# Kernel tuning notes

Measured on AMD Instinct MI355X. Metric: run time of the kernel, lower is better.

Reference implementation:

```python
import math
import jax, jax.numpy as jnp
import numpy as np

L, H, D, FF, V, S = 12, 12, 768, 3072, 32000, 1024
HD = D // H
EPS = 1e-5
B, T = 2, 1024


def layernorm(x, w, b):
    mu = jnp.mean(x, axis=-1, keepdims=True)
    var = jnp.mean(jnp.square(x - mu), axis=-1, keepdims=True)
    return (x - mu) * jax.lax.rsqrt(var + EPS) * w + b


def setup_inputs() -> dict:
    key = jax.random.key(0)
    ks = jax.random.split(key, 12)
    std = 0.02
    std_res = 0.02 / math.sqrt(2 * L)  # out_proj / down_proj scaled init
    return {
        "input_ids": jax.random.randint(ks[0], (B, T), 0, V),
        "tok_emb": jax.random.normal(ks[1], (V, D), jnp.float32) * std,
        "pos_emb": jax.random.normal(ks[2], (S, D), jnp.float32) * std,
        "ln1_w": jnp.ones((L, D), jnp.float32),
        "ln1_b": jnp.zeros((L, D), jnp.float32),
        "qkv_w": jax.random.normal(ks[3], (L, 3 * D, D), jnp.float32) * std,
        "out_w": jax.random.normal(ks[4], (L, D, D), jnp.float32) * std_res,
        "ln2_w": jnp.ones((L, D), jnp.float32),
        "ln2_b": jnp.zeros((L, D), jnp.float32),
        "up_w": jax.random.normal(ks[5], (L, FF, D), jnp.float32) * std,
        "down_w": jax.random.normal(ks[6], (L, D, FF), jnp.float32) * std_res,
        "lnf_w": jnp.ones((D,), jnp.float32),
        "lnf_b": jnp.zeros((D,), jnp.float32),
    }


def reference(input_ids, tok_emb, pos_emb, ln1_w, ln1_b, qkv_w, out_w,
              ln2_w, ln2_b, up_w, down_w, lnf_w, lnf_b):
    b, t = input_ids.shape
    x = tok_emb[input_ids] + pos_emb[:t]  # (B,T,D); dropout = eval no-op
    causal = jnp.tril(jnp.ones((t, t), bool))  # (T,T)
    scale = 1.0 / math.sqrt(HD)

    def block(x, p):
        l1w, l1b, qkvw, ow, l2w, l2b, uw, dw = p
        h = layernorm(x, l1w, l1b)
        qkv = h @ qkvw.T  # (B,T,3D)
        q, k, v = jnp.split(qkv, 3, axis=-1)
        q = q.reshape(b, t, H, HD)
        k = k.reshape(b, t, H, HD)
        v = v.reshape(b, t, H, HD)
        scores = jnp.einsum('bihd,bjhd->bhij', q, k) * scale
        scores = jnp.where(causal, scores, -jnp.inf)
        probs = jax.nn.softmax(scores, axis=-1)  # attn_dropout = eval no-op
        o = jnp.einsum('bhij,bjhd->bihd', probs, v).reshape(b, t, D)
        x = x + o @ ow.T
        h2 = layernorm(x, l2w, l2b)
        x = x + jax.nn.gelu(h2 @ uw.T, approximate=False) @ dw.T
        return x, None

    x, _ = jax.lax.scan(block, x, (ln1_w, ln1_b, qkv_w, out_w, ln2_w, ln2_b, up_w, down_w))
    x = layernorm(x, lnf_w, lnf_b)
    logits = x @ tok_emb.T  # tied lm_head
    return logits
```

## Files before the change

kernel.cpp:

```cpp
#include <hip/hip_runtime.h>
#include <hip/hip_bf16.h>
#include <math.h>

#define L_  12
#define H_  12
#define D_  768
#define FF_ 3072
#define V_  32000
#define T_  1024
#define B_  2
#define BT_ (B_*T_)

typedef unsigned short ushort_t;
typedef unsigned int   uint_t;
typedef __bf16 bf16x8 __attribute__((ext_vector_type(8)));
typedef float  f32x4  __attribute__((ext_vector_type(4)));

__device__ __forceinline__ uint_t f2bf1(float f) {
    uint_t u = __builtin_bit_cast(uint_t, f);
    return (u + 0x7FFFu + ((u >> 16) & 1u)) >> 16;
}
__device__ __forceinline__ uint_t f2bf2(float lo, float hi) {
    return f2bf1(lo) | (f2bf1(hi) << 16);
}

__device__ __forceinline__ void gl_lds16(const ushort_t* g, ushort_t* l) {
    __builtin_amdgcn_global_load_lds(
        (const __attribute__((address_space(1))) uint_t*)g,
        (__attribute__((address_space(3))) uint_t*)l, 16, 0, 0);
}

__global__ __launch_bounds__(256) void cast_bf16(const float* __restrict__ in,
                                                 ushort_t* __restrict__ out, int n8)
{
    for (int i = blockIdx.x * 256 + threadIdx.x; i < n8; i += gridDim.x * 256) {
        const float4* p = (const float4*)(in + (size_t)i * 8);
        float4 a = p[0], b = p[1];
        *(uint4*)(out + (size_t)i * 8) =
            make_uint4(f2bf2(a.x,a.y), f2bf2(a.z,a.w), f2bf2(b.x,b.y), f2bf2(b.z,b.w));
    }
}

#define EPI_F32   0
#define EPI_BF16  1
#define EPI_GELU  2
#define EPI_PART  3

template <int EPI, int BM, int KS>
__global__ __launch_bounds__(256) void gemm_bt(
    const ushort_t* __restrict__ A, const ushort_t* __restrict__ W,
    const float* R, void* Cv, int N, int K, int Kc)
{
    constexpr int MI = BM / 32;
    constexpr int AH = BM * 32;
    constexpr int BH = 128 * 32;
    __shared__ ushort_t As[2 * AH];
    __shared__ ushort_t Bs[2 * BH];

    const int tid  = threadIdx.x;
    const int w    = tid >> 6;
    const int lane = tid & 63;

    const int nwg = gridDim.x;
    int swz = (blockIdx.x & 7) * (nwg >> 3) + (blockIdx.x >> 3);
    constexpr int MT = 2048 / BM;
    const int mt = swz & (MT - 1);
    int rest     = swz / MT;
    const int ks = rest & (KS - 1);
    const int nt = rest / KS;
    const int m0 = mt * BM, n0 = nt * 128;
    const int kb = ks * Kc;

    const int srow = lane >> 2;
    const int scol = ((lane & 3) ^ ((srow >> 1) & 3)) * 8;
    const ushort_t* gA = A + (size_t)(m0 + w * (BM / 4) + srow) * K + scol;
    const ushort_t* gW = W + (size_t)(n0 + w * 32 + srow) * K + scol;
    const size_t row16 = (size_t)16 * K;

    const int lr = lane & 15;
    const int lg = lane >> 4;
    const int wm = (w >> 1) * (BM / 2);
    const int wn = (w & 1) * 64;

    f32x4 acc[MI][4] = {};

    auto stage = [&](int buf, int k0) {
        ushort_t* lA = As + buf * AH + w * (BM / 4) * 32;
        ushort_t* lB = Bs + buf * BH + w * 1024;
        #pragma unroll
        for (int i = 0; i < BM / 64; ++i)
            gl_lds16(gA + k0 + i * row16, lA + i * 512);
        #pragma unroll
        for (int i = 0; i < 2; ++i)
            gl_lds16(gW + k0 + i * row16, lB + i * 512);
    };

    stage(0, kb);
    __syncthreads();
    int cur = 0;
    for (int k0 = kb; k0 < kb + Kc; k0 += 32) {
        if (k0 + 32 < kb + Kc) stage(cur ^ 1, k0 + 32);
        const ushort_t* Ab = As + cur * AH;
        const ushort_t* Bb = Bs + cur * BH;
        __builtin_amdgcn_s_setprio(1);
        {
            bf16x8 av[MI], bv[4];
            #pragma unroll
            for (int i = 0; i < MI; ++i) {
                int rr = wm + i * 16 + lr;
                int ch = lg ^ ((rr >> 1) & 3);
                av[i] = *(const bf16x8*)&Ab[rr * 32 + ch * 8];
            }
            #pragma unroll
            for (int j = 0; j < 4; ++j) {
                int rr = wn + j * 16 + lr;
                int ch = lg ^ ((rr >> 1) & 3);
                bv[j] = *(const bf16x8*)&Bb[rr * 32 + ch * 8];
            }
            #pragma unroll
            for (int i = 0; i < MI; ++i)
                #pragma unroll
                for (int j = 0; j < 4; ++j)
                    acc[i][j] = __builtin_amdgcn_mfma_f32_16x16x32_bf16(av[i], bv[j], acc[i][j], 0, 0, 0);
        }
        __builtin_amdgcn_s_setprio(0);
        __syncthreads();
        cur ^= 1;
    }

    float*    Cf = (float*)Cv;
    ushort_t* Cb = (ushort_t*)Cv;
    float*    Pp = (EPI == EPI_PART) ? (ks ? const_cast<float*>(R) : (float*)Cv) : nullptr;
    const int rbase = lg * 4;
    #pragma unroll
    for (int i = 0; i < MI; ++i) {
        #pragma unroll
        for (int j = 0; j < 4; ++j) {
            #pragma unroll
            for (int r = 0; r < 4; ++r) {
                int row = m0 + wm + i * 16 + rbase + r;
                int col = n0 + wn + j * 16 + lr;
                size_t idx = (size_t)row * N + col;
                float v = acc[i][j][r];
                if (EPI == EPI_F32)  Cf[idx] = v;
                if (EPI == EPI_BF16) Cb[idx] = (ushort_t)f2bf1(v);
                if (EPI == EPI_GELU) Cb[idx] = (ushort_t)f2bf1(0.5f * v * (1.0f + erff(v * 0.70710678118654752f)));
                if (EPI == EPI_PART) Pp[idx] = v;
            }
        }
    }
}

__global__ __launch_bounds__(256) void vprep(const ushort_t* __restrict__ qkv,
                                             ushort_t* __restrict__ vt)
{
    __shared__ ushort_t Vs[64][72];
    const int blk   = blockIdx.x;
    const int ttile = blk & 15;
    const int bh    = blk >> 4;
    const int b     = bh / H_;
    const int h     = bh % H_;
    const int tid   = threadIdx.x;
    const int t0    = ttile * 64;
    {
        const int tr = tid >> 2;
        const int dc = (tid & 3) * 16;
        const uint4* src = (const uint4*)(qkv + (size_t)(b * T_ + t0 + tr) * 2304 + 1536 + h * 64 + dc);
        uint4 v0 = src[0], v1 = src[1];
        *(uint4*)&Vs[tr][dc]     = v0;
        *(uint4*)&Vs[tr][dc + 8] = v1;
    }
    __syncthreads();
    {
        const int d  = tid >> 2;
        const int jc = (tid & 3) * 16;
        uint_t w[8];
        #pragma unroll
        for (int i = 0; i < 8; ++i)
            w[i] = (uint_t)Vs[jc + 2*i][d] | ((uint_t)Vs[jc + 2*i + 1][d] << 16);
        uint4* dst = (uint4*)(vt + ((size_t)bh * 64 + d) * T_ + t0 + jc);
        dst[0] = make_uint4(w[0], w[1], w[2], w[3]);
        dst[1] = make_uint4(w[4], w[5], w[6], w[7]);
    }
}

__global__ __launch_bounds__(64) void attn_mfma(const ushort_t* __restrict__ qkv,
    const ushort_t* __restrict__ vt, ushort_t* __restrict__ o)
{
    __shared__ ushort_t Ps[16 * 136];

    int swz = (blockIdx.x & 7) * 192 + (blockIdx.x >> 3);
    const int bh  = swz >> 6;
    const int qtl = 63 - (swz & 63);
    const int b   = bh / H_;
    const int h   = bh % H_;
    const int lane = threadIdx.x;
    const int l15  = lane & 15;
    const int lg   = lane >> 4;
    const int qbase = qtl * 16;
    const int qlast = qbase + 15;

    const ushort_t* qp = qkv + ((size_t)(b * T_) + qbase + l15) * 2304 + h * 64 + lg * 8;
    bf16x8 qf0 = *(const bf16x8*)qp;
    bf16x8 qf1 = *(const bf16x8*)(qp + 32);

    f32x4 od[4] = {};
    float mr[4] = {-INFINITY, -INFINITY, -INFINITY, -INFINITY};
    float lr[4] = {0.f, 0.f, 0.f, 0.f};

    const ushort_t* kbase = qkv + (size_t)(b * T_) * 2304 + 768 + h * 64;
    const ushort_t* vbase = vt + (size_t)bh * 64 * T_;
    const float SC = 0.18033688011112042f;

    for (int j0 = 0; j0 <= qlast; j0 += 128) {
        f32x4 s[8];
        __builtin_amdgcn_s_setprio(1);
        #pragma unroll
        for (int n = 0; n < 8; ++n) {
            if (j0 + 16 * n <= qlast) {
                const ushort_t* kr = kbase + (size_t)(j0 + 16 * n + l15) * 2304 + lg * 8;
                bf16x8 kf0 = *(const bf16x8*)kr;
                bf16x8 kf1 = *(const bf16x8*)(kr + 32);
                f32x4 a = {};
                a = __builtin_amdgcn_mfma_f32_16x16x32_bf16(qf0, kf0, a, 0, 0, 0);
                a = __builtin_amdgcn_mfma_f32_16x16x32_bf16(qf1, kf1, a, 0, 0, 0);
                s[n] = a;
            } else {
                s[n] = f32x4{-INFINITY, -INFINITY, -INFINITY, -INFINITY};
            }
        }
        __builtin_amdgcn_s_setprio(0);

        #pragma unroll
        for (int n = 0; n < 8; ++n) {
            #pragma unroll
            for (int r = 0; r < 4; ++r) {
                float v = s[n][r] * SC;
                int jg = j0 + 16 * n + l15;
                int qg = qbase + lg * 4 + r;
                if (jg > qg) v = -INFINITY;
                s[n][r] = v;
            }
        }

        float al[4];
        #pragma unroll
        for (int r = 0; r < 4; ++r) {
            float tm = fmaxf(fmaxf(fmaxf(s[0][r], s[1][r]), fmaxf(s[2][r], s[3][r])),
                             fmaxf(fmaxf(s[4][r], s[5][r]), fmaxf(s[6][r], s[7][r])));
            tm = fmaxf(tm, __shfl_xor(tm, 1, 64));
            tm = fmaxf(tm, __shfl_xor(tm, 2, 64));
            tm = fmaxf(tm, __shfl_xor(tm, 4, 64));
            tm = fmaxf(tm, __shfl_xor(tm, 8, 64));
            float mn = fmaxf(mr[r], tm);
            al[r] = exp2f(mr[r] - mn);
            mr[r] = mn;
        }
        #pragma unroll
        for (int n = 0; n < 8; ++n)
            #pragma unroll
            for (int r = 0; r < 4; ++r)
                s[n][r] = exp2f(s[n][r] - mr[r]);
        #pragma unroll
        for (int r = 0; r < 4; ++r) {
            float ps = (s[0][r] + s[1][r]) + (s[2][r] + s[3][r]);
            ps += (s[4][r] + s[5][r]) + (s[6][r] + s[7][r]);
            ps += __shfl_xor(ps, 1, 64);
            ps += __shfl_xor(ps, 2, 64);
            ps += __shfl_xor(ps, 4, 64);
            ps += __shfl_xor(ps, 8, 64);
            lr[r] = lr[r] * al[r] + ps;
        }
        #pragma unroll
        for (int n = 0; n < 4; ++n)
            #pragma unroll
            for (int r = 0; r < 4; ++r)
                od[n][r] *= al[r];

        #pragma unroll
        for (int n = 0; n < 8; ++n)
            #pragma unroll
            for (int r = 0; r < 4; ++r)
                Ps[(lg * 4 + r) * 136 + 16 * n + l15] = (ushort_t)f2bf1(s[n][r]);

        __builtin_amdgcn_s_setprio(1);
        #pragma unroll
        for (int kc = 0; kc < 4; ++kc) {
            if (j0 + kc * 32 <= qlast) {
                bf16x8 pa = *(const bf16x8*)&Ps[l15 * 136 + kc * 32 + lg * 8];
                #pragma unroll
                for (int nn = 0; nn < 4; ++nn) {
                    bf16x8 vf = *(const bf16x8*)&vbase[(size_t)(16 * nn + l15) * T_ + j0 + kc * 32 + lg * 8];
                    od[nn] = __builtin_amdgcn_mfma_f32_16x16x32_bf16(pa, vf, od[nn], 0, 0, 0);
                }
            }
        }
        __builtin_amdgcn_s_setprio(0);
    }

    #pragma unroll
    for (int r = 0; r < 4; ++r) {
        float inv = 1.0f / lr[r];
        int row = qbase + lg * 4 + r;
        ushort_t* op = o + ((size_t)(b * T_ + row)) * 768 + h * 64 + l15;
        #pragma unroll
        for (int nn = 0; nn < 4; ++nn)
            op[16 * nn] = (ushort_t)f2bf1(od[nn][r] * inv);
    }
}

__global__ __launch_bounds__(256) void ln_kernel(const float* __restrict__ x,
    const float* __restrict__ w, const float* __restrict__ bia, ushort_t* __restrict__ out)
{
    const int row = blockIdx.x;
    const int tid = threadIdx.x;
    const float* xr = x + (size_t)row * 768;
    float v0 = xr[tid], v1 = xr[tid + 256], v2 = xr[tid + 512];
    float s  = v0 + v1 + v2;
    float s2 = v0 * v0 + v1 * v1 + v2 * v2;
    #pragma unroll
    for (int off = 32; off > 0; off >>= 1) {
        s  += __shfl_down(s,  off, 64);
        s2 += __shfl_down(s2, off, 64);
    }
    __shared__ float sh[8];
    const int wave = tid >> 6;
    if ((tid & 63) == 0) { sh[wave] = s; sh[4 + wave] = s2; }
    __syncthreads();
    float S  = sh[0] + sh[1] + sh[2] + sh[3];
    float S2 = sh[4] + sh[5] + sh[6] + sh[7];
    float mean = S * (1.f / 768.f);
    float var  = S2 * (1.f / 768.f) - mean * mean;
    float inv  = rsqrtf(var + 1e-5f);
    ushort_t* orow = out + (size_t)row * 768;
    orow[tid]       = (ushort_t)f2bf1((v0 - mean) * inv * w[tid]       + bia[tid]);
    orow[tid + 256] = (ushort_t)f2bf1((v1 - mean) * inv * w[tid + 256] + bia[tid + 256]);
    orow[tid + 512] = (ushort_t)f2bf1((v2 - mean) * inv * w[tid + 512] + bia[tid + 512]);
}

__global__ __launch_bounds__(256) void ln_red(float* __restrict__ x,
    const float* __restrict__ P0, const float* __restrict__ P1,
    const float* __restrict__ w, const float* __restrict__ bia, ushort_t* __restrict__ out)
{
    const int row = blockIdx.x;
    const int tid = threadIdx.x;
    const size_t base = (size_t)row * 768;
    float v0 = x[base + tid]       + P0[base + tid]       + P1[base + tid];
    float v1 = x[base + tid + 256] + P0[base + tid + 256] + P1[base + tid + 256];
    float v2 = x[base + tid + 512] + P0[base + tid + 512] + P1[base + tid + 512];
    x[base + tid]       = v0;
    x[base + tid + 256] = v1;
    x[base + tid + 512] = v2;
    float s  = v0 + v1 + v2;
    float s2 = v0 * v0 + v1 * v1 + v2 * v2;
    #pragma unroll
    for (int off = 32; off > 0; off >>= 1) {
        s  += __shfl_down(s,  off, 64);
        s2 += __shfl_down(s2, off, 64);
    }
    __shared__ float sh[8];
    const int wave = tid >> 6;
    if ((tid & 63) == 0) { sh[wave] = s; sh[4 + wave] = s2; }
    __syncthreads();
    float S  = sh[0] + sh[1] + sh[2] + sh[3];
    float S2 = sh[4] + sh[5] + sh[6] + sh[7];
    float mean = S * (1.f / 768.f);
    float var  = S2 * (1.f / 768.f) - mean * mean;
    float inv  = rsqrtf(var + 1e-5f);
    ushort_t* orow = out + base;
    orow[tid]       = (ushort_t)f2bf1((v0 - mean) * inv * w[tid]       + bia[tid]);
    orow[tid + 256] = (ushort_t)f2bf1((v1 - mean) * inv * w[tid + 256] + bia[tid + 256]);
    orow[tid + 512] = (ushort_t)f2bf1((v2 - mean) * inv * w[tid + 512] + bia[tid + 512]);
}

__global__ __launch_bounds__(256) void embed_kernel(const int* __restrict__ ids,
    const float* __restrict__ tok, const float* __restrict__ pos, float* __restrict__ x)
{
    const int bt = blockIdx.x;
    const int t  = bt % T_;
    const int id = ids[bt];
    const int tid = threadIdx.x;
    const float* tr = tok + (size_t)id * 768;
    const float* pr = pos + (size_t)t * 768;
    float* xr = x + (size_t)bt * 768;
    xr[tid]       = tr[tid]       + pr[tid];
    xr[tid + 256] = tr[tid + 256] + pr[tid + 256];
    xr[tid + 512] = tr[tid + 512] + pr[tid + 512];
}

extern "C" void kernel_launch(void* const* d_in, const int* in_sizes, int n_in,
                              void* d_out, int out_size, void* d_ws, size_t ws_size,
                              hipStream_t stream)
{
    const int*   ids   = (const int*)  d_in[0];
    const float* tok   = (const float*)d_in[1];
    const float* pos   = (const float*)d_in[2];
    const float* ln1w  = (const float*)d_in[3];
    const float* ln1b  = (const float*)d_in[4];
    const float* qkvw  = (const float*)d_in[5];
    const float* outw  = (const float*)d_in[6];
    const float* ln2w  = (const float*)d_in[7];
    const float* ln2b  = (const float*)d_in[8];
    const float* upw   = (const float*)d_in[9];
    const float* downw = (const float*)d_in[10];
    const float* lnfw  = (const float*)d_in[11];
    const float* lnfb  = (const float*)d_in[12];
    float* out = (float*)d_out;

    char* ws = (char*)d_ws;
    ushort_t* h    = (ushort_t*)ws;
    float*    x    = (float*)   (ws + 3145728);
    ushort_t* qkv  = (ushort_t*)(ws + 9437184);
    ushort_t* o    = qkv  + (size_t)BT_ * 3 * D_;
    ushort_t* vt   = o    + (size_t)BT_ * D_;
    ushort_t* ffh  = vt   + (size_t)B_ * H_ * 64 * T_;
    float*    Pa   = (float*)(ws + 37748736);
    float*    Pb   = (float*)(ws + 44040192);
    ushort_t* qkvwB  = (ushort_t*)(ws + 50331648);
    ushort_t* outwB  = qkvwB  + (size_t)L_ * 3 * D_ * D_;
    ushort_t* upwB   = outwB  + (size_t)L_ * D_ * D_;
    ushort_t* downwB = upwB   + (size_t)L_ * FF_ * D_;
    ushort_t* tokW   = downwB + (size_t)L_ * D_ * FF_;

    cast_bf16<<<2048, 256, 0, stream>>>(qkvw,  qkvwB,  L_ * 3 * D_ * D_ / 8);
    cast_bf16<<<2048, 256, 0, stream>>>(outw,  outwB,  L_ * D_ * D_ / 8);
    cast_bf16<<<2048, 256, 0, stream>>>(upw,   upwB,   L_ * FF_ * D_ / 8);
    cast_bf16<<<2048, 256, 0, stream>>>(downw, downwB, L_ * D_ * FF_ / 8);

    embed_kernel<<<BT_, 256, 0, stream>>>(ids, tok, pos, x);

    for (int l = 0; l < L_; ++l) {
        if (l == 0)
            ln_kernel<<<BT_, 256, 0, stream>>>(x, ln1w, ln1b, h);
        else
            ln_red<<<BT_, 256, 0, stream>>>(x, Pa, Pb, ln1w + l * D_, ln1b + l * D_, h);

        gemm_bt<EPI_BF16, 128, 1><<<16 * (3 * D_ / 128), 256, 0, stream>>>(
            h, qkvwB + (size_t)l * 3 * D_ * D_, nullptr, qkv, 3 * D_, D_, D_);

        vprep<<<B_ * H_ * (T_ / 64), 256, 0, stream>>>(qkv, vt);
        attn_mfma<<<B_ * H_ * (T_ / 16), 64, 0, stream>>>(qkv, vt, o);

        gemm_bt<EPI_PART, 64, 2><<<32 * (D_ / 128) * 2, 256, 0, stream>>>(
            o, outwB + (size_t)l * D_ * D_, Pb, Pa, D_, D_, D_ / 2);

        ln_red<<<BT_, 256, 0, stream>>>(x, Pa, Pb, ln2w + l * D_, ln2b + l * D_, h);

        gemm_bt<EPI_GELU, 128, 1><<<16 * (FF_ / 128), 256, 0, stream>>>(
            h, upwB + (size_t)l * FF_ * D_, nullptr, ffh, FF_, D_, D_);

        gemm_bt<EPI_PART, 64, 2><<<32 * (D_ / 128) * 2, 256, 0, stream>>>(
            ffh, downwB + (size_t)l * D_ * FF_, Pb, Pa, D_, FF_, FF_ / 2);
    }

    ln_red<<<BT_, 256, 0, stream>>>(x, Pa, Pb, lnfw, lnfb, h);

    cast_bf16<<<2048, 256, 0, stream>>>(tok, tokW, V_ * D_ / 8);
    gemm_bt<EPI_F32, 128, 1><<<16 * (V_ / 128), 256, 0, stream>>>(
        h, tokW, nullptr, out, V_, D_, D_);
}
```

Measured before the change: 2.234 ms.

## Fuse V transpose into QKV GEMM epilogue and cast weights per layer

The QKV GEMM gains an epilogue that writes Q and K row-major and scatters V directly into the transposed per-head layout, which removes the separate vprep kernel and its round trip through memory. The four large upfront weight casts become one fused per-layer cast into a small reused buffer, so the bf16 weights of each layer are likely still in L2 when the GEMMs read them. The QKV and up-projection GEMMs switch from BM=128 to BM=64 tiles, doubling the grid. The risks are scattered 8-byte V stores, an extra launch per layer, and more weight re-reads with smaller tiles.

After: 2.036 ms. 1.1x faster.

```diff
diff --git a/kernel.cpp b/kernel.cpp
--- a/kernel.cpp
+++ b/kernel.cpp
@@ -41,15 +41,34 @@
     }
 }
 
+__global__ __launch_bounds__(256) void cast_layer(const float* __restrict__ q,
+    const float* __restrict__ o, const float* __restrict__ u, const float* __restrict__ d,
+    ushort_t* __restrict__ out)
+{
+    const int N0 = 3*D_*D_/8, N1 = N0 + D_*D_/8, N2 = N1 + FF_*D_/8, N3 = N2 + D_*FF_/8;
+    for (int i = blockIdx.x * 256 + threadIdx.x; i < N3; i += gridDim.x * 256) {
+        const float* src;
+        if      (i < N0) src = q + (size_t)i * 8;
+        else if (i < N1) src = o + (size_t)(i - N0) * 8;
+        else if (i < N2) src = u + (size_t)(i - N1) * 8;
+        else             src = d + (size_t)(i - N2) * 8;
+        const float4* p = (const float4*)src;
+        float4 a = p[0], b = p[1];
+        *(uint4*)(out + (size_t)i * 8) =
+            make_uint4(f2bf2(a.x,a.y), f2bf2(a.z,a.w), f2bf2(b.x,b.y), f2bf2(b.z,b.w));
+    }
+}
+
 #define EPI_F32   0
 #define EPI_BF16  1
 #define EPI_GELU  2
 #define EPI_PART  3
+#define EPI_QKV   4
 
 template <int EPI, int BM, int KS>
 __global__ __launch_bounds__(256) void gemm_bt(
     const ushort_t* __restrict__ A, const ushort_t* __restrict__ W,
-    const float* R, void* Cv, int N, int K, int Kc)
+    const float* R, void* Cv, ushort_t* __restrict__ Vt, int N, int K, int Kc)
 {
     constexpr int MI = BM / 32;
     constexpr int AH = BM * 32;
@@ -136,51 +155,33 @@
     for (int i = 0; i < MI; ++i) {
         #pragma unroll
         for (int j = 0; j < 4; ++j) {
-            #pragma unroll
-            for (int r = 0; r < 4; ++r) {
-                int row = m0 + wm + i * 16 + rbase + r;
-                int col = n0 + wn + j * 16 + lr;
-                size_t idx = (size_t)row * N + col;
-                float v = acc[i][j][r];
-                if (EPI == EPI_F32)  Cf[idx] = v;
-                if (EPI == EPI_BF16) Cb[idx] = (ushort_t)f2bf1(v);
-                if (EPI == EPI_GELU) Cb[idx] = (ushort_t)f2bf1(0.5f * v * (1.0f + erff(v * 0.70710678118654752f)));
-                if (EPI == EPI_PART) Pp[idx] = v;
-            }
-        }
-    }
-}
-
-__global__ __launch_bounds__(256) void vprep(const ushort_t* __restrict__ qkv,
-                                             ushort_t* __restrict__ vt)
-{
-    __shared__ ushort_t Vs[64][72];
-    const int blk   = blockIdx.x;
-    const int ttile = blk & 15;
-    const int bh    = blk >> 4;
-    const int b     = bh / H_;
-    const int h     = bh % H_;
-    const int tid   = threadIdx.x;
-    const int t0    = ttile * 64;
-    {
-        const int tr = tid >> 2;
-        const int dc = (tid & 3) * 16;
-        const uint4* src = (const uint4*)(qkv + (size_t)(b * T_ + t0 + tr) * 2304 + 1536 + h * 64 + dc);
-        uint4 v0 = src[0], v1 = src[1];
-        *(uint4*)&Vs[tr][dc]     = v0;
-        *(uint4*)&Vs[tr][dc + 8] = v1;
-    }
-    __syncthreads();
-    {
-        const int d  = tid >> 2;
-        const int jc = (tid & 3) * 16;
-        uint_t w[8];
-        #pragma unroll
-        for (int i = 0; i < 8; ++i)
-            w[i] = (uint_t)Vs[jc + 2*i][d] | ((uint_t)Vs[jc + 2*i + 1][d] << 16);
-        uint4* dst = (uint4*)(vt + ((size_t)bh * 64 + d) * T_ + t0 + jc);
-        dst[0] = make_uint4(w[0], w[1], w[2], w[3]);
-        dst[1] = make_uint4(w[4], w[5], w[6], w[7]);
+            const int row0 = m0 + wm + i * 16 + rbase;
+            const int col  = n0 + wn + j * 16 + lr;
+            if (EPI == EPI_QKV) {
+                if (col < 1536) {
+                    #pragma unroll
+                    for (int r = 0; r < 4; ++r)
+                        Cb[(size_t)(row0 + r) * 2304 + col] = (ushort_t)f2bf1(acc[i][j][r]);
+                } else {
+                    const int hh = (col - 1536) >> 6, dd = (col - 1536) & 63;
+                    const int bb = row0 >> 10,        tt = row0 & 1023;
+                    uint2 pk;
+                    pk.x = f2bf2(acc[i][j][0], acc[i][j][1]);
+                    pk.y = f2bf2(acc[i][j][2], acc[i][j][3]);
+                    *(uint2*)&Vt[(((size_t)bb * H_ + hh) * 64 + dd) * T_ + tt] = pk;
+                }
+            } else {
+                #pragma unroll
+                for (int r = 0; r < 4; ++r) {
+                    size_t idx = (size_t)(row0 + r) * N + col;
+                    float v = acc[i][j][r];
+                    if (EPI == EPI_F32)  Cf[idx] = v;
+                    if (EPI == EPI_BF16) Cb[idx] = (ushort_t)f2bf1(v);
+                    if (EPI == EPI_GELU) Cb[idx] = (ushort_t)f2bf1(0.5f * v * (1.0f + erff(v * 0.70710678118654752f)));
+                    if (EPI == EPI_PART) Pp[idx] = v;
+                }
+            }
+        }
     }
 }
 
@@ -416,46 +417,48 @@
     ushort_t* ffh  = vt   + (size_t)B_ * H_ * 64 * T_;
     float*    Pa   = (float*)(ws + 37748736);
     float*    Pb   = (float*)(ws + 44040192);
-    ushort_t* qkvwB  = (ushort_t*)(ws + 50331648);
-    ushort_t* outwB  = qkvwB  + (size_t)L_ * 3 * D_ * D_;
-    ushort_t* upwB   = outwB  + (size_t)L_ * D_ * D_;
-    ushort_t* downwB = upwB   + (size_t)L_ * FF_ * D_;
-    ushort_t* tokW   = downwB + (size_t)L_ * D_ * FF_;
-
-    cast_bf16<<<2048, 256, 0, stream>>>(qkvw,  qkvwB,  L_ * 3 * D_ * D_ / 8);
-    cast_bf16<<<2048, 256, 0, stream>>>(outw,  outwB,  L_ * D_ * D_ / 8);
-    cast_bf16<<<2048, 256, 0, stream>>>(upw,   upwB,   L_ * FF_ * D_ / 8);
-    cast_bf16<<<2048, 256, 0, stream>>>(downw, downwB, L_ * D_ * FF_ / 8);
+    ushort_t* layerW = (ushort_t*)(ws + 50331648);
+    ushort_t* tokW   = (ushort_t*)(ws + 67108864);
+
+    ushort_t* qkvwB  = layerW;
+    ushort_t* outwB  = qkvwB + (size_t)3 * D_ * D_;
+    ushort_t* upwB   = outwB + (size_t)D_ * D_;
+    ushort_t* downwB = upwB  + (size_t)FF_ * D_;
 
     embed_kernel<<<BT_, 256, 0, stream>>>(ids, tok, pos, x);
 
     for (int l = 0; l < L_; ++l) {
+        cast_layer<<<1024, 256, 0, stream>>>(
+            qkvw  + (size_t)l * 3 * D_ * D_,
+            outw  + (size_t)l * D_ * D_,
+            upw   + (size_t)l * FF_ * D_,
+            downw + (size_t)l * D_ * FF_, layerW);
+
         if (l == 0)
             ln_kernel<<<BT_, 256, 0, stream>>>(x, ln1w, ln1b, h);
         else
             ln_red<<<BT_, 256, 0, stream>>>(x, Pa, Pb, ln1w + l * D_, ln1b + l * D_, h);
 
-        gemm_bt<EPI_BF16, 128, 1><<<16 * (3 * D_ / 128), 256, 0, stream>>>(
-            h, qkvwB + (size_t)l * 3 * D_ * D_, nullptr, qkv, 3 * D_, D_, D_);
-
-        vprep<<<B_ * H_ * (T_ / 64), 256, 0, stream>>>(qkv, vt);
+        gemm_bt<EPI_QKV, 64, 1><<<32 * (3 * D_ / 128), 256, 0, stream>>>(
+            h, qkvwB, nullptr, qkv, vt, 3 * D_, D_, D_);
+
         attn_mfma<<<B_ * H_ * (T_ / 16), 64, 0, stream>>>(qkv, vt, o);
 
         gemm_bt<EPI_PART, 64, 2><<<32 * (D_ / 128) * 2, 256, 0, stream>>>(
-            o, outwB + (size_t)l * D_ * D_, Pb, Pa, D_, D_, D_ / 2);
+            o, outwB, Pb, Pa, nullptr, D_, D_, D_ / 2);
 
         ln_red<<<BT_, 256, 0, stream>>>(x, Pa, Pb, ln2w + l * D_, ln2b + l * D_, h);
 
-        gemm_bt<EPI_GELU, 128, 1><<<16 * (FF_ / 128), 256, 0, stream>>>(
-            h, upwB + (size_t)l * FF_ * D_, nullptr, ffh, FF_, D_, D_);
+        gemm_bt<EPI_GELU, 64, 1><<<32 * (FF_ / 128), 256, 0, stream>>>(
+            h, upwB, nullptr, ffh, nullptr, FF_, D_, D_);
 
         gemm_bt<EPI_PART, 64, 2><<<32 * (D_ / 128) * 2, 256, 0, stream>>>(
-            ffh, downwB + (size_t)l * D_ * FF_, Pb, Pa, D_, FF_, FF_ / 2);
+            ffh, downwB, Pb, Pa, nullptr, D_, FF_, FF_ / 2);
     }
 
     ln_red<<<BT_, 256, 0, stream>>>(x, Pa, Pb, lnfw, lnfb, h);
 
     cast_bf16<<<2048, 256, 0, stream>>>(tok, tokW, V_ * D_ / 8);
     gemm_bt<EPI_F32, 128, 1><<<16 * (V_ / 128), 256, 0, stream>>>(
-        h, tokW, nullptr, out, V_, D_, D_);
-}
+        h, tokW, nullptr, out, nullptr, V_, D_, D_);
+}
```
